# Performance work log

Measured on AMD Instinct MI355X. Metric: run time of the kernel, lower is better.

The kernel has to match this reference:

```python
import jax, jax.numpy as jnp
import numpy as np

B, D_IN, D_OUT = 8192, 512, 1024
N_PATHS, N_STEPS = 256, 50  # n_paths = min(output_size, 256); n_steps fixed at 50
T_HORIZON, DECAY_RATE = 1.0, 0.1


def setup_inputs() -> dict:
    key = jax.random.key(0)
    k_x, k_wfb, k_wagg, k_noise = jax.random.split(key, 4)
    x = jax.random.normal(k_x, (B, D_IN), dtype=jnp.float32)
    W_fb = jax.random.normal(k_wfb, (1, D_IN), dtype=jnp.float32) / np.sqrt(D_IN)
    b_fb = jnp.zeros((1,), dtype=jnp.float32)
    W_agg = jax.random.normal(k_wagg, (D_OUT, N_PATHS), dtype=jnp.float32) / np.sqrt(N_PATHS)
    b_agg = jnp.zeros((D_OUT,), dtype=jnp.float32)
    # Pre-drawn standard normal increments for all batch items / paths / steps
    noise = jax.random.normal(k_noise, (B, N_PATHS, N_STEPS), dtype=jnp.float32)
    return {"x": x, "W_fb": W_fb, "b_fb": b_fb, "W_agg": W_agg, "b_agg": b_agg, "noise": noise}


def reference(x, W_fb, b_fb, W_agg, b_agg, noise):
    # feedback_transform + sigmoid -> scalar feedback per sample  [B]
    feedback = jax.nn.sigmoid(x @ W_fb.T + b_fb)[:, 0]
    # original extracts feedback via .item(): no grad flows into the simulation
    fb = jax.lax.stop_gradient(feedback)

    dt = jnp.asarray(T_HORIZON / N_STEPS, dtype=x.dtype)
    t = jnp.arange(N_STEPS, dtype=x.dtype) * dt                 # [S]
    # per-sample, per-step drift-free diffusion scale: 0.5 + fb * exp(-decay * t)
    scale = 0.5 + fb[:, None] * jnp.exp(-DECAY_RATE * t)[None, :]  # [B, S]

    # endpoint of X_{t+1} = X_t + sqrt(dt) * scale_t * noise_t, X_0 = 0
    # == sqrt(dt) * sum_t scale[b,t] * noise[b,p,t]
    endpoints = jnp.einsum('bps,bs->bp', noise, scale) * jnp.sqrt(dt)  # [B, P]

    # path_aggregator linear
    return endpoints @ W_agg.T + b_agg  # [B, D_OUT]
```

## Files before the change

kernel.cpp:

```cpp
#include <hip/hip_runtime.h>
#include <math.h>


#define B_TOTAL 8192
#define D_IN    512
#define D_OUT   1024
#define NP      256
#define NS      50
#define BT      16
#define THREADS 256
#define PCHUNK  8
#define NCHUNK  (NP / PCHUNK)
#define CHUNK_F4 1600
#define ROW_F4   100
#define EP_STRIDE 264

#define SQRT_DT 0.14142135623730951f

typedef __bf16 bf16x8 __attribute__((ext_vector_type(8)));
typedef float  f32x4  __attribute__((ext_vector_type(4)));

__device__ __forceinline__ unsigned short f2bf(float f) {
    unsigned u = __float_as_uint(f);
    return (unsigned short)((u + 0x7FFFu + ((u >> 16) & 1u)) >> 16);
}

__global__ __launch_bounds__(THREADS, 2) void bicep_main(
    const float* __restrict__ x,
    const float* __restrict__ Wfb,
    const float* __restrict__ bfb,
    const float* __restrict__ Wagg,
    const float* __restrict__ bagg,
    const float* __restrict__ noise,
    float* __restrict__ out)
{
    __shared__ __align__(16) float nbuf[2][CHUNK_F4 * 4];
    __shared__ __align__(16) unsigned short ep_bf[BT * EP_STRIDE];
    __shared__ float fb_s[BT];
    __shared__ float bagg_s[D_OUT];

    const int tid  = threadIdx.x;
    const int lane = tid & 63;
    const int wave = tid >> 6;
    const int b0   = blockIdx.x * BT;

    {
        #pragma unroll
        for (int i = 0; i < D_OUT / THREADS; ++i)
            bagg_s[i * THREADS + tid] = bagg[i * THREADS + tid];

        const float bf_b = bfb[0];
        const float4* wf = (const float4*)Wfb + lane * 2;
        float4 wa = wf[0], wb = wf[1];
        #pragma unroll
        for (int rr = 0; rr < 4; ++rr) {
            int row = wave * 4 + rr;
            const float4* xr = (const float4*)(x + (size_t)(b0 + row) * D_IN) + lane * 2;
            float4 xa = xr[0], xb = xr[1];
            float p = xa.x*wa.x + xa.y*wa.y + xa.z*wa.z + xa.w*wa.w
                    + xb.x*wb.x + xb.y*wb.y + xb.z*wb.z + xb.w*wb.w;
            #pragma unroll
            for (int mm = 32; mm >= 1; mm >>= 1) p += __shfl_xor(p, mm, 64);
            if (lane == 0) fb_s[row] = 1.0f / (1.0f + __expf(-(p + bf_b)));
        }
    }

    const int h     = tid & 1;
    const int jpair = tid >> 1;
    const int c_row = jpair >> 3;
    const int c_pl  = jpair & 7;

    float ereg[25];
    #pragma unroll
    for (int s = 0; s < 25; ++s)
        ereg[s] = __expf(-0.002f * (float)(h * 25 + s));

    const float4* nptr[7];
    #pragma unroll
    for (int r = 0; r < 7; ++r) {
        int g4  = r * 256 + tid;
        int row = g4 / 100;
        int off = g4 - row * 100;
        if (row > BT - 1) row = BT - 1;
        nptr[r] = (const float4*)(noise + (size_t)(b0 + row) * (NP * NS)) + off;
    }

    float4 v[7];
    v[6] = make_float4(0.f, 0.f, 0.f, 0.f);
    #pragma unroll
    for (int r = 0; r < 6; ++r) v[r] = nptr[r][0];
    if (tid < 64) v[6] = nptr[6][0];

    for (int c = 0; c < NCHUNK; ++c) {
        float* nb = nbuf[c & 1];
        #pragma unroll
        for (int r = 0; r < 6; ++r) ((float4*)nb)[r * 256 + tid] = v[r];
        if (tid < 64) ((float4*)nb)[6 * 256 + tid] = v[6];

        if (c + 1 < NCHUNK) {
            #pragma unroll
            for (int r = 0; r < 6; ++r) v[r] = nptr[r][(c + 1) * ROW_F4];
            if (tid < 64) v[6] = nptr[6][(c + 1) * ROW_F4];
        }

        __syncthreads();

        const float* src = &nb[c_row * (PCHUNK * NS) + c_pl * NS + h * 25];
        float s0 = 0.f, s1 = 0.f;
        #pragma unroll
        for (int s = 0; s < 25; ++s) {
            float nv = src[s];
            s0 += nv;
            s1 = fmaf(ereg[s], nv, s1);
        }
        s0 += __shfl_xor(s0, 1, 64);
        s1 += __shfl_xor(s1, 1, 64);
        if (h == 0) {
            float ep = SQRT_DT * fmaf(fb_s[c_row], s1, 0.5f * s0);
            ep_bf[c_row * EP_STRIDE + c * PCHUNK + c_pl] = f2bf(ep);
        }
    }
    __syncthreads();

    {
        const int m  = lane & 15;
        const int kg = lane >> 4;

        bf16x8 afr[8];
        #pragma unroll
        for (int ks = 0; ks < 8; ++ks)
            afr[ks] = *(const bf16x8*)&ep_bf[m * EP_STRIDE + ks * 32 + kg * 8];

        #pragma unroll 2
        for (int i = 0; i < 16; ++i) {
            int O = wave * 16 + i;
            const float* wp = Wagg + (size_t)(O * 16 + m) * NP + kg * 8;
            f32x4 acc = {0.f, 0.f, 0.f, 0.f};
            #pragma unroll
            for (int ks = 0; ks < 8; ++ks) {
                float4 wa = *(const float4*)(wp + ks * 32);
                float4 wb = *(const float4*)(wp + ks * 32 + 4);
                bf16x8 bfr = { (__bf16)wa.x, (__bf16)wa.y, (__bf16)wa.z, (__bf16)wa.w,
                               (__bf16)wb.x, (__bf16)wb.y, (__bf16)wb.z, (__bf16)wb.w };
                acc = __builtin_amdgcn_mfma_f32_16x16x32_bf16(afr[ks], bfr, acc, 0, 0, 0);
            }
            float bias = bagg_s[O * 16 + m];
            #pragma unroll
            for (int r = 0; r < 4; ++r)
                out[(size_t)(b0 + kg * 4 + r) * D_OUT + O * 16 + m] = acc[r] + bias;
        }
    }
}

extern "C" void kernel_launch(void* const* d_in, const int* in_sizes, int n_in,
                              void* d_out, int out_size, void* d_ws, size_t ws_size,
                              hipStream_t stream) {
    const float* x     = (const float*)d_in[0];
    const float* Wfb   = (const float*)d_in[1];
    const float* bfb   = (const float*)d_in[2];
    const float* Wagg  = (const float*)d_in[3];
    const float* bagg  = (const float*)d_in[4];
    const float* noise = (const float*)d_in[5];
    float* out = (float*)d_out;
    (void)d_ws; (void)ws_size;

    bicep_main<<<dim3(B_TOTAL / BT), dim3(THREADS), 0, stream>>>(
        x, Wfb, bfb, Wagg, bagg, noise, out);
}
```

Measured before the change: 668.6 us.

## Give each wave its own noise staging buffer and use Horner decay sums

Each wave now streams the noise rows of its own four batch samples into a private LDS stage. This removes the block-wide __syncthreads per chunk and the 7-row cross-wave split. Each lane reduces a whole 50-step path with float2 loads, evaluating the exponential-decay weighted sum by Horner recurrence instead of a 25-entry register table and a shuffle reduction. Within a wave there is no double buffering, so the write-then-read to the stage relies on wave-level ordering. Lane reads at a stride of 50 floats may cause LDS bank conflicts.

```diff
diff --git a/kernel.cpp b/kernel.cpp
--- a/kernel.cpp
+++ b/kernel.cpp
@@ -9,13 +9,11 @@
 #define NS      50
 #define BT      16
 #define THREADS 256
-#define PCHUNK  8
-#define NCHUNK  (NP / PCHUNK)
-#define CHUNK_F4 1600
-#define ROW_F4   100
 #define EP_STRIDE 264
 
 #define SQRT_DT 0.14142135623730951f
+#define G_STEP  0.99800199866f
+#define G_STEP2 0.99600798935f
 
 typedef __bf16 bf16x8 __attribute__((ext_vector_type(8)));
 typedef float  f32x4  __attribute__((ext_vector_type(4)));
@@ -34,7 +32,7 @@
     const float* __restrict__ noise,
     float* __restrict__ out)
 {
-    __shared__ __align__(16) float nbuf[2][CHUNK_F4 * 4];
+    __shared__ __align__(16) float4 stage[4][800];
     __shared__ __align__(16) unsigned short ep_bf[BT * EP_STRIDE];
     __shared__ float fb_s[BT];
     __shared__ float bagg_s[D_OUT];
@@ -65,59 +63,41 @@
         }
     }
 
-    const int h     = tid & 1;
-    const int jpair = tid >> 1;
-    const int c_row = jpair >> 3;
-    const int c_pl  = jpair & 7;
+    {
+        float4* st = stage[wave];
+        const float4* base = (const float4*)noise + (size_t)(b0 + wave * 4) * 3200;
 
-    float ereg[25];
-    #pragma unroll
-    for (int s = 0; s < 25; ++s)
-        ereg[s] = __expf(-0.002f * (float)(h * 25 + s));
-
-    const float4* nptr[7];
-    #pragma unroll
-    for (int r = 0; r < 7; ++r) {
-        int g4  = r * 256 + tid;
-        int row = g4 / 100;
-        int off = g4 - row * 100;
-        if (row > BT - 1) row = BT - 1;
-        nptr[r] = (const float4*)(noise + (size_t)(b0 + row) * (NP * NS)) + off;
-    }
-
-    float4 v[7];
-    v[6] = make_float4(0.f, 0.f, 0.f, 0.f);
-    #pragma unroll
-    for (int r = 0; r < 6; ++r) v[r] = nptr[r][0];
-    if (tid < 64) v[6] = nptr[6][0];
-
-    for (int c = 0; c < NCHUNK; ++c) {
-        float* nb = nbuf[c & 1];
-        #pragma unroll
-        for (int r = 0; r < 6; ++r) ((float4*)nb)[r * 256 + tid] = v[r];
-        if (tid < 64) ((float4*)nb)[6 * 256 + tid] = v[6];
-
-        if (c + 1 < NCHUNK) {
+        float4 v[13];
+        {
+            const float4* p0 = base;
             #pragma unroll
-            for (int r = 0; r < 6; ++r) v[r] = nptr[r][(c + 1) * ROW_F4];
-            if (tid < 64) v[6] = nptr[6][(c + 1) * ROW_F4];
+            for (int i = 0; i < 12; ++i) v[i] = p0[i * 64 + lane];
+            v[12] = p0[768 + (lane & 31)];
         }
 
-        __syncthreads();
+        for (int c = 0; c < 16; ++c) {
+            #pragma unroll
+            for (int i = 0; i < 12; ++i) st[i * 64 + lane] = v[i];
+            st[768 + (lane & 31)] = v[12];
 
-        const float* src = &nb[c_row * (PCHUNK * NS) + c_pl * NS + h * 25];
-        float s0 = 0.f, s1 = 0.f;
-        #pragma unroll
-        for (int s = 0; s < 25; ++s) {
-            float nv = src[s];
-            s0 += nv;
-            s1 = fmaf(ereg[s], nv, s1);
-        }
-        s0 += __shfl_xor(s0, 1, 64);
-        s1 += __shfl_xor(s1, 1, 64);
-        if (h == 0) {
-            float ep = SQRT_DT * fmaf(fb_s[c_row], s1, 0.5f * s0);
-            ep_bf[c_row * EP_STRIDE + c * PCHUNK + c_pl] = f2bf(ep);
+            if (c + 1 < 16) {
+                const float4* pn = base + (size_t)(c + 1) * 800;
+                #pragma unroll
+                for (int i = 0; i < 12; ++i) v[i] = pn[i * 64 + lane];
+                v[12] = pn[768 + (lane & 31)];
+            }
+
+            const float2* run = (const float2*)((const float*)st + lane * 50);
+            float s0 = 0.f, t1 = 0.f;
+            #pragma unroll
+            for (int j = 24; j >= 0; --j) {
+                float2 n2 = run[j];
+                s0 += n2.x + n2.y;
+                t1 = fmaf(t1, G_STEP2, fmaf(n2.y, G_STEP, n2.x));
+            }
+            const int lr = wave * 4 + (c >> 2);
+            float ep = SQRT_DT * fmaf(fb_s[lr], t1, 0.5f * s0);
+            ep_bf[lr * EP_STRIDE + (c & 3) * 64 + lane] = f2bf(ep);
         }
     }
     __syncthreads();
```

After: 673.0 us. About the same (+0.6%).
